# Performance work log

Measured on AMD Instinct MI355X. Metric: run time of the kernel, lower is better.

## Reference

```python
import jax, jax.numpy as jnp
import numpy as np

N, E, F_IN, H, C = 50000, 800000, 128, 64, 10

def setup_inputs() -> dict:
    key = jax.random.key(0)
    ks = jax.random.split(key, 8)
    x = jax.random.normal(ks[0], (N, F_IN), dtype=jnp.float32)
    edge_index = jax.random.randint(ks[1], (2, E), 0, N, dtype=jnp.int32)
    edge_weight = jax.random.uniform(ks[2], (E,), dtype=jnp.float32)
    W1 = jax.random.normal(ks[3], (H, F_IN), dtype=jnp.float32) * 0.05
    W2 = jax.random.normal(ks[4], (H, H), dtype=jnp.float32) * 0.05
    W3 = jax.random.normal(ks[5], (C, H), dtype=jnp.float32) * 0.05
    b1 = jnp.zeros((H,), jnp.float32)
    b2 = jnp.zeros((H,), jnp.float32)
    b3 = jnp.zeros((C,), jnp.float32)
    return {"x": x, "edge_index": edge_index, "edge_weight": edge_weight,
            "W1": W1, "b1": b1, "W2": W2, "b2": b2, "W3": W3, "b3": b3}

def reference(x, edge_index, edge_weight, W1, b1, W2, b2, W3, b3):
    n = x.shape[0]
    row, col = edge_index[0], edge_index[1]
    # GCN symmetric normalization (add_self_loops=False): deg from edge weights on col
    deg = jax.ops.segment_sum(edge_weight, col, num_segments=n)  # [N]
    dinv = jnp.where(deg > 0, jax.lax.rsqrt(deg), 0.0)
    norm = dinv[row] * edge_weight * dinv[col]  # [E]

    def gcn_layer(h, W, b):
        h = h @ W.T                               # linear transform [N, out]
        msg = h[row] * norm[:, None]              # gather + scale   [E, out]
        agg = jax.ops.segment_sum(msg, col, num_segments=n)  # scatter-add [N, out]
        return agg + b

    h = gcn_layer(x, W1, b1)
    h = gcn_layer(h, W2, b2)
    logits = gcn_layer(h, W3, b3)
    soft = jax.nn.softmax(logits, axis=1)
    return logits, soft
```

## Files before the change

kernel.cpp:

```cpp
#include <hip/hip_runtime.h>
#include <hip/hip_fp16.h>

#define N_NODES 50000
#define N_EDGES 800000
#define F_IN    128
#define H_DIM   64
#define C_DIM   10
#define CPAD    16
#define CAP     48
#define BLOCK   256
#define BIN_NODES 256
#define NBINS   196
#define QN      64
#define STRIDE  4480
#define E_BLK   2048
#define ABLOCKS ((N_EDGES + E_BLK - 1) / E_BLK)
#define GBLK    2048
#define NWAVES  (GBLK * 4)
#define POISON  ((int)0xAAAAAAAA)

__device__ __forceinline__ int unbase(int v) {
    return ((unsigned)v < 65536u) ? v : v - POISON;
}

__device__ __forceinline__ int   prow(unsigned v) { return (int)(v >> 16); }
__device__ __forceinline__ float pw(unsigned v)   {
    return __half2float(__ushort_as_half((unsigned short)(v & 0xFFFFu)));
}

__global__ __launch_bounds__(256) void k_binA(const int* __restrict__ rows,
                                              const int* __restrict__ cols,
                                              const float* __restrict__ ew,
                                              const float* __restrict__ W1,
                                              const float* __restrict__ b1,
                                              const float* __restrict__ W2,
                                              const float* __restrict__ b2,
                                              const float* __restrict__ W3,
                                              int* __restrict__ bucketCnt,
                                              unsigned* __restrict__ regionA,
                                              unsigned short* __restrict__ regionC,
                                              float* __restrict__ T2g,
                                              float* __restrict__ v1g,
                                              float* __restrict__ v2g) {
    const int tid = threadIdx.x;
    if (blockIdx.x < ABLOCKS) {
        __shared__ unsigned       sA[E_BLK];
        __shared__ unsigned short sC[E_BLK];
        __shared__ int hcnt[NBINS];
        __shared__ int lbase[NBINS];
        __shared__ int gb[NBINS];
        for (int i = tid; i < NBINS; i += BLOCK) hcnt[i] = 0;
        __syncthreads();

        const int e0 = blockIdx.x * E_BLK;
        unsigned rw[8];
        unsigned cl[8];
#pragma unroll
        for (int j = 0; j < 8; ++j) {
            int e = e0 + j * BLOCK + tid;
            if (e < N_EDGES) {
                int   c = cols[e];
                int   r = rows[e];
                float w = ew[e];
                rw[j] = ((unsigned)r << 16) | (unsigned)__half_as_ushort(__float2half(w));
                int lr = atomicAdd(&hcnt[c >> 8], 1);
                cl[j] = (unsigned)c | ((unsigned)lr << 16);
            } else {
                cl[j] = 0xFFFFFFFFu;
            }
        }
        __syncthreads();

        if (tid < 64) {
            int run = 0;
            for (int base = 0; base < NBINS; base += 64) {
                int i = base + tid;
                int v = (i < NBINS) ? hcnt[i] : 0;
                int s = v;
#pragma unroll
                for (int off = 1; off < 64; off <<= 1) {
                    int t = __shfl_up(s, off);
                    if (tid >= off) s += t;
                }
                if (i < NBINS) lbase[i] = run + s - v;
                run += __shfl(s, 63);
            }
        }
        __syncthreads();

#pragma unroll
        for (int j = 0; j < 8; ++j) {
            if (cl[j] != 0xFFFFFFFFu) {
                int c  = (int)(cl[j] & 0xFFFFu);
                int lr = (int)(cl[j] >> 16);
                int pos = lbase[c >> 8] + lr;
                sA[pos] = rw[j];
                sC[pos] = (unsigned short)c;
            }
        }
        if (tid < NBINS && hcnt[tid] > 0)
            gb[tid] = unbase(atomicAdd(&bucketCnt[tid], hcnt[tid]));
        __syncthreads();

        const int total = lbase[NBINS - 1] + hcnt[NBINS - 1];
        for (int i = tid; i < total; i += BLOCK) {
            int c = sC[i];
            int b = c >> 8;
            int gpos = gb[b] + (i - lbase[b]);
            if (gpos < STRIDE) {
                size_t p = (size_t)b * STRIDE + gpos;
                regionA[p] = sA[i];
                regionC[p] = (unsigned short)c;
            }
        }
        return;
    }

    __shared__ float u[C_DIM * H_DIM];
    for (int idx = tid; idx < C_DIM * H_DIM; idx += BLOCK) {
        int c = idx >> 6, j = idx & 63;
        float a = 0.f;
#pragma unroll
        for (int k = 0; k < H_DIM; ++k) a += W3[c * H_DIM + k] * W2[k * H_DIM + j];
        u[idx] = a;
    }
    __syncthreads();
    for (int idx = tid; idx < C_DIM * F_IN; idx += BLOCK) {
        int c = idx >> 7, f = idx & 127;
        float a = 0.f;
#pragma unroll
        for (int k = 0; k < H_DIM; ++k) a += u[c * H_DIM + k] * W1[k * F_IN + f];
        T2g[idx] = a;
    }
    if (tid < C_DIM) {
        float a = 0.f, b = 0.f;
#pragma unroll
        for (int k = 0; k < H_DIM; ++k) {
            a += u[tid * H_DIM + k] * b1[k];
            b += W3[tid * H_DIM + k] * b2[k];
        }
        v1g[tid] = a;
        v2g[tid] = b;
    }
}

__global__ __launch_bounds__(256) void k_binB(const int* __restrict__ bucketCnt,
                                              const unsigned* __restrict__ regionA,
                                              const unsigned short* __restrict__ regionC,
                                              const float* __restrict__ x,
                                              const float* __restrict__ T2g,
                                              float2* __restrict__ meta,
                                              unsigned* __restrict__ edata,
                                              __half* __restrict__ bufA) {
    __shared__ unsigned sdata[QN * CAP];
    __shared__ int   lcnt[QN];
    __shared__ float wsum[QN];
    __shared__ float dinvs[QN];
    __shared__ float ts[16 * 132];
    __shared__ float xs[16][132];
    const int tid = threadIdx.x;
    const int b   = blockIdx.x >> 2;
    const int q   = blockIdx.x & 3;
    const int n0  = b * BIN_NODES + q * QN;
    if (n0 >= N_NODES) return;
    if (tid < QN) { lcnt[tid] = 0; wsum[tid] = 0.f; }
    for (int i = tid; i < 16 * F_IN; i += BLOCK) {
        int c = i >> 7;
        ts[c * 132 + (i & 127)] = (c < C_DIM) ? T2g[i] : 0.f;
    }
    __syncthreads();

    int tot = unbase(bucketCnt[b]);
    if (tot > STRIDE) tot = STRIDE;
    const size_t segBase = (size_t)b * STRIDE;
    const int lo = q * QN, hi = lo + QN;
    for (int i = tid; i < tot; i += BLOCK) {
        int cl = (int)regionC[segBase + i] - b * BIN_NODES;
        unsigned e = regionA[segBase + i];
        if (cl >= lo && cl < hi) {
            int nl = cl - lo;
            int r = atomicAdd(&lcnt[nl], 1);
            if (r < CAP) sdata[nl * CAP + r] = e;
            atomicAdd(&wsum[nl], pw(e));
        }
    }
    __syncthreads();

    const int nvalid = min(N_NODES - n0, QN);
    if (tid < nvalid) {
        int c0 = min(lcnt[tid], CAP);
        int cp = (c0 + 15) & ~15;
        if (cp > CAP) cp = CAP;
        for (int r = c0; r < cp; ++r) sdata[tid * CAP + r] = 0u;
        float d = wsum[tid];
        float di = d > 0.f ? rsqrtf(d) : 0.f;
        dinvs[tid] = di;
        meta[n0 + tid] = make_float2(di, (float)cp);
    }
    __syncthreads();

    {
        int4* dst = reinterpret_cast<int4*>(edata + (size_t)n0 * CAP);
        const int4* src = reinterpret_cast<const int4*>(sdata);
        const int nvec = nvalid * (CAP / 4);
        for (int i = tid; i < nvec; i += BLOCK) dst[i] = src[i];
    }

    const int g = tid >> 4, c = tid & 15;
    for (int t = 0; t < QN / 16; ++t) {
        __syncthreads();
        const int n0t = n0 + t * 16;
        for (int i = tid; i < 16 * 32; i += BLOCK) {
            int ln = i >> 5, f4 = i & 31;
            if (n0t + ln < N_NODES) {
                float4 v = reinterpret_cast<const float4*>(x)[(n0t + ln) * 32 + f4];
                *reinterpret_cast<float4*>(&xs[ln][f4 * 4]) = v;
            }
        }
        __syncthreads();
        const int n = n0t + g;
        if (n < N_NODES) {
            const float di = dinvs[t * 16 + g];
            const float4* tsv = reinterpret_cast<const float4*>(&ts[c * 132]);
            const float4* xv  = reinterpret_cast<const float4*>(&xs[g][0]);
            float a = 0.f;
#pragma unroll 8
            for (int f4 = 0; f4 < 32; ++f4) {
                float4 xx = xv[f4], tt = tsv[f4];
                a += xx.x * tt.x + xx.y * tt.y + xx.z * tt.z + xx.w * tt.w;
            }
            float outv = (c < C_DIM) ? a * di : (c == 10 ? di : 0.f);
            bufA[n * CPAD + c] = __float2half(outv);
        }
    }
}

__global__ __launch_bounds__(256) void k_gather(const float2* __restrict__ meta,
                                                const unsigned* __restrict__ edata,
                                                const __half* __restrict__ zin,
                                                __half* __restrict__ zout) {
    const int lane = threadIdx.x & 63;
    const int sub = lane >> 3;
    const int c2  = lane & 7;
    const int w0 = (blockIdx.x * 256 + threadIdx.x) >> 6;
    for (int n = w0; n < N_NODES; n += NWAVES) {
        float2 m = meta[n];
        const float di = m.x;
        const int iters = ((int)m.y) >> 4;
        const uint2* bp = reinterpret_cast<const uint2*>(edata + n * CAP) + sub;
        float ax = 0.f, ay = 0.f;
#pragma unroll
        for (int i = 0; i < 3; ++i) {
            if (i < iters) {
                uint2 e = bp[i * 8];
                {
                    float2 z = __half22float2(
                        reinterpret_cast<const __half2*>(zin + prow(e.x) * CPAD)[c2]);
                    float w = pw(e.x);
                    ax += w * z.x; ay += w * z.y;
                }
                {
                    float2 z = __half22float2(
                        reinterpret_cast<const __half2*>(zin + prow(e.y) * CPAD)[c2]);
                    float w = pw(e.y);
                    ax += w * z.x; ay += w * z.y;
                }
            }
        }
        ax += __shfl_xor(ax, 8);  ay += __shfl_xor(ay, 8);
        ax += __shfl_xor(ax, 16); ay += __shfl_xor(ay, 16);
        ax += __shfl_xor(ax, 32); ay += __shfl_xor(ay, 32);
        if (lane < 8) {
            float s = di * di;
            reinterpret_cast<__half2*>(zout + n * CPAD)[lane] =
                __floats2half2_rn(ax * s, ay * s);
        }
    }
}

__global__ __launch_bounds__(256) void k_final(const float2* __restrict__ meta,
                                               const unsigned* __restrict__ edata,
                                               const __half* __restrict__ zin,
                                               const __half* __restrict__ s1buf,
                                               const float* __restrict__ v1,
                                               const float* __restrict__ v2,
                                               const float* __restrict__ b3,
                                               float* __restrict__ logits,
                                               float* __restrict__ soft) {
    const int lane = threadIdx.x & 63;
    const int sub = lane >> 3;
    const int c2  = lane & 7;
    const int w0 = (blockIdx.x * 256 + threadIdx.x) >> 6;
    for (int n = w0; n < N_NODES; n += NWAVES) {
        float2 m = meta[n];
        const float di = m.x;
        const int iters = ((int)m.y) >> 4;
        const uint2* bp = reinterpret_cast<const uint2*>(edata + n * CAP) + sub;
        float ax = 0.f, ay = 0.f;
#pragma unroll
        for (int i = 0; i < 3; ++i) {
            if (i < iters) {
                uint2 e = bp[i * 8];
                {
                    float2 z = __half22float2(
                        reinterpret_cast<const __half2*>(zin + prow(e.x) * CPAD)[c2]);
                    float w = pw(e.x);
                    ax += w * z.x; ay += w * z.y;
                }
                {
                    float2 z = __half22float2(
                        reinterpret_cast<const __half2*>(zin + prow(e.y) * CPAD)[c2]);
                    float w = pw(e.y);
                    ax += w * z.x; ay += w * z.y;
                }
            }
        }
        ax += __shfl_xor(ax, 8);  ay += __shfl_xor(ay, 8);
        ax += __shfl_xor(ax, 16); ay += __shfl_xor(ay, 16);
        ax += __shfl_xor(ax, 32); ay += __shfl_xor(ay, 32);

        const float r  = di > 0.f ? 1.0f / di : 0.f;
        const float a1 = __half2float(s1buf[n * CPAD + 10]) * r;
        const float a2 = __half2float(zin[n * CPAD + 10]) * r;
        float l0 = -1e30f, l1 = -1e30f;
        if (c2 < 5) {
            float2 w1 = reinterpret_cast<const float2*>(v1)[c2];
            float2 w2 = reinterpret_cast<const float2*>(v2)[c2];
            float2 bb = reinterpret_cast<const float2*>(b3)[c2];
            l0 = di * ax + a2 * w1.x + a1 * w2.x + bb.x;
            l1 = di * ay + a2 * w1.y + a1 * w2.y + bb.y;
        }
        float mx = fmaxf(l0, l1);
        mx = fmaxf(mx, __shfl_xor(mx, 1));
        mx = fmaxf(mx, __shfl_xor(mx, 2));
        mx = fmaxf(mx, __shfl_xor(mx, 4));
        float e0 = (c2 < 5) ? __expf(l0 - mx) : 0.f;
        float e1 = (c2 < 5) ? __expf(l1 - mx) : 0.f;
        float s = e0 + e1;
        s += __shfl_xor(s, 1);
        s += __shfl_xor(s, 2);
        s += __shfl_xor(s, 4);
        if (lane < 5) {
            float inv = 1.0f / s;
            reinterpret_cast<float2*>(logits + (size_t)n * C_DIM)[lane] = make_float2(l0, l1);
            reinterpret_cast<float2*>(soft   + (size_t)n * C_DIM)[lane] = make_float2(e0 * inv, e1 * inv);
        }
    }
}

extern "C" void kernel_launch(void* const* d_in, const int* in_sizes, int n_in,
                              void* d_out, int out_size, void* d_ws, size_t ws_size,
                              hipStream_t stream) {
    const float* x  = (const float*)d_in[0];
    const int*   ei = (const int*)d_in[1];
    const float* ew = (const float*)d_in[2];
    const float* W1 = (const float*)d_in[3];
    const float* b1 = (const float*)d_in[4];
    const float* W2 = (const float*)d_in[5];
    const float* b2 = (const float*)d_in[6];
    const float* W3 = (const float*)d_in[7];
    const float* b3 = (const float*)d_in[8];
    const int* rows = ei;
    const int* cols = ei + N_EDGES;

    char* ws = (char*)d_ws;
    size_t off = 0;
    auto alloc = [&](size_t bytes) { void* q = ws + off; off += (bytes + 15) & ~size_t(15); return q; };

    float2*         meta      = (float2*)         alloc((size_t)N_NODES * 8);
    __half*         bufA      = (__half*)         alloc((size_t)N_NODES * CPAD * 2);
    __half*         bufB      = (__half*)         alloc((size_t)N_NODES * CPAD * 2);
    float*          T2g       = (float*)          alloc(C_DIM * F_IN * 4);
    float*          v1        = (float*)          alloc(64);
    float*          v2        = (float*)          alloc(64);
    int*            bucketCnt = (int*)            alloc(NBINS * 4);
    unsigned*       regionA   = (unsigned*)       alloc((size_t)NBINS * STRIDE * 4);
    unsigned short* regionC   = (unsigned short*) alloc((size_t)NBINS * STRIDE * 2);
    unsigned*       edata     = (unsigned*)       alloc((size_t)N_NODES * CAP * 4);

    float* logits = (float*)d_out;
    float* soft   = logits + N_NODES * C_DIM;

    k_binA<<<ABLOCKS + 1, BLOCK, 0, stream>>>(rows, cols, ew, W1, b1, W2, b2, W3,
                                              bucketCnt, regionA, regionC, T2g, v1, v2);
    k_binB<<<NBINS * 4, BLOCK, 0, stream>>>(bucketCnt, regionA, regionC, x, T2g,
                                            meta, edata, bufA);
    k_gather<<<GBLK, BLOCK, 0, stream>>>(meta, edata, bufA, bufB);
    k_gather<<<GBLK, BLOCK, 0, stream>>>(meta, edata, bufB, bufA);
    k_final<<<GBLK, BLOCK, 0, stream>>>(meta, edata, bufA, bufB, v1, v2, b3,
                                        logits, soft);
}
```

Measured before the change: 163.0 us.

## Bin edges directly into 64-node sub-buckets to avoid redundant bucket scans

The edge binning pass now partitions edges into 782 buckets of 64 destination nodes instead of 196 buckets of 256 nodes, using a block-wide scan over the larger histogram. Each binB block then reads only its own bucket rather than scanning a 256-node bucket and discarding three quarters of the entries, which cuts the redundant regionA/regionC reads by four times. In exchange the per-block histogram, scan and global atomics in binA grow roughly fourfold, and the smaller per-bucket capacity of 1280 raises the risk of overflow on skewed degree distributions.

```diff
diff --git a/kernel.cpp b/kernel.cpp
--- a/kernel.cpp
+++ b/kernel.cpp
@@ -9,10 +9,9 @@
 #define CPAD    16
 #define CAP     48
 #define BLOCK   256
-#define BIN_NODES 256
-#define NBINS   196
 #define QN      64
-#define STRIDE  4480
+#define NSUB    ((N_NODES + QN - 1) / QN)
+#define SSTRIDE 1280
 #define E_BLK   2048
 #define ABLOCKS ((N_EDGES + E_BLK - 1) / E_BLK)
 #define GBLK    2048
@@ -46,10 +45,11 @@
     if (blockIdx.x < ABLOCKS) {
         __shared__ unsigned       sA[E_BLK];
         __shared__ unsigned short sC[E_BLK];
-        __shared__ int hcnt[NBINS];
-        __shared__ int lbase[NBINS];
-        __shared__ int gb[NBINS];
-        for (int i = tid; i < NBINS; i += BLOCK) hcnt[i] = 0;
+        __shared__ int hcnt[NSUB];
+        __shared__ int lbase[NSUB];
+        __shared__ int gb[NSUB];
+        __shared__ int wtot[4];
+        for (int i = tid; i < NSUB; i += BLOCK) hcnt[i] = 0;
         __syncthreads();
 
         const int e0 = blockIdx.x * E_BLK;
@@ -63,7 +63,7 @@
                 int   r = rows[e];
                 float w = ew[e];
                 rw[j] = ((unsigned)r << 16) | (unsigned)__half_as_ushort(__float2half(w));
-                int lr = atomicAdd(&hcnt[c >> 8], 1);
+                int lr = atomicAdd(&hcnt[c >> 6], 1);
                 cl[j] = (unsigned)c | ((unsigned)lr << 16);
             } else {
                 cl[j] = 0xFFFFFFFFu;
@@ -71,21 +71,30 @@
         }
         __syncthreads();
 
-        if (tid < 64) {
-            int run = 0;
-            for (int base = 0; base < NBINS; base += 64) {
-                int i = base + tid;
-                int v = (i < NBINS) ? hcnt[i] : 0;
-                int s = v;
-#pragma unroll
-                for (int off = 1; off < 64; off <<= 1) {
-                    int t = __shfl_up(s, off);
-                    if (tid >= off) s += t;
-                }
-                if (i < NBINS) lbase[i] = run + s - v;
-                run += __shfl(s, 63);
-            }
-        }
+        const int lane = tid & 63, wid = tid >> 6;
+        const int b4 = tid << 2;
+        int h0 = (b4 + 0 < NSUB) ? hcnt[b4 + 0] : 0;
+        int h1 = (b4 + 1 < NSUB) ? hcnt[b4 + 1] : 0;
+        int h2 = (b4 + 2 < NSUB) ? hcnt[b4 + 2] : 0;
+        int h3 = (b4 + 3 < NSUB) ? hcnt[b4 + 3] : 0;
+        int ls = h0 + h1 + h2 + h3;
+        int incl = ls;
+#pragma unroll
+        for (int off = 1; off < 64; off <<= 1) {
+            int t = __shfl_up(incl, off);
+            if (lane >= off) incl += t;
+        }
+        if (lane == 63) wtot[wid] = incl;
+        __syncthreads();
+        int woff = 0;
+#pragma unroll
+        for (int w = 0; w < 4; ++w) if (w < wid) woff += wtot[w];
+        int run = woff + incl - ls;
+        if (b4 + 0 < NSUB) { lbase[b4 + 0] = run; run += h0; }
+        if (b4 + 1 < NSUB) { lbase[b4 + 1] = run; run += h1; }
+        if (b4 + 2 < NSUB) { lbase[b4 + 2] = run; run += h2; }
+        if (b4 + 3 < NSUB) { lbase[b4 + 3] = run; run += h3; }
+        const int total = wtot[0] + wtot[1] + wtot[2] + wtot[3];
         __syncthreads();
 
 #pragma unroll
@@ -93,22 +102,21 @@
             if (cl[j] != 0xFFFFFFFFu) {
                 int c  = (int)(cl[j] & 0xFFFFu);
                 int lr = (int)(cl[j] >> 16);
-                int pos = lbase[c >> 8] + lr;
+                int pos = lbase[c >> 6] + lr;
                 sA[pos] = rw[j];
                 sC[pos] = (unsigned short)c;
             }
         }
-        if (tid < NBINS && hcnt[tid] > 0)
-            gb[tid] = unbase(atomicAdd(&bucketCnt[tid], hcnt[tid]));
-        __syncthreads();
-
-        const int total = lbase[NBINS - 1] + hcnt[NBINS - 1];
+        for (int i = tid; i < NSUB; i += BLOCK)
+            if (hcnt[i] > 0) gb[i] = unbase(atomicAdd(&bucketCnt[i], hcnt[i]));
+        __syncthreads();
+
         for (int i = tid; i < total; i += BLOCK) {
             int c = sC[i];
-            int b = c >> 8;
-            int gpos = gb[b] + (i - lbase[b]);
-            if (gpos < STRIDE) {
-                size_t p = (size_t)b * STRIDE + gpos;
+            int s = c >> 6;
+            int gpos = gb[s] + (i - lbase[s]);
+            if (gpos < SSTRIDE) {
+                size_t p = (size_t)s * SSTRIDE + gpos;
                 regionA[p] = sA[i];
                 regionC[p] = (unsigned short)c;
             }
@@ -159,9 +167,8 @@
     __shared__ float ts[16 * 132];
     __shared__ float xs[16][132];
     const int tid = threadIdx.x;
-    const int b   = blockIdx.x >> 2;
-    const int q   = blockIdx.x & 3;
-    const int n0  = b * BIN_NODES + q * QN;
+    const int s   = blockIdx.x;
+    const int n0  = s * QN;
     if (n0 >= N_NODES) return;
     if (tid < QN) { lcnt[tid] = 0; wsum[tid] = 0.f; }
     for (int i = tid; i < 16 * F_IN; i += BLOCK) {
@@ -170,19 +177,15 @@
     }
     __syncthreads();
 
-    int tot = unbase(bucketCnt[b]);
-    if (tot > STRIDE) tot = STRIDE;
-    const size_t segBase = (size_t)b * STRIDE;
-    const int lo = q * QN, hi = lo + QN;
+    int tot = unbase(bucketCnt[s]);
+    if (tot > SSTRIDE) tot = SSTRIDE;
+    const size_t segBase = (size_t)s * SSTRIDE;
     for (int i = tid; i < tot; i += BLOCK) {
-        int cl = (int)regionC[segBase + i] - b * BIN_NODES;
         unsigned e = regionA[segBase + i];
-        if (cl >= lo && cl < hi) {
-            int nl = cl - lo;
-            int r = atomicAdd(&lcnt[nl], 1);
-            if (r < CAP) sdata[nl * CAP + r] = e;
-            atomicAdd(&wsum[nl], pw(e));
-        }
+        int nl = (int)regionC[segBase + i] & (QN - 1);
+        int r = atomicAdd(&lcnt[nl], 1);
+        if (r < CAP) sdata[nl * CAP + r] = e;
+        atomicAdd(&wsum[nl], pw(e));
     }
     __syncthreads();
 
@@ -271,9 +274,9 @@
         ax += __shfl_xor(ax, 16); ay += __shfl_xor(ay, 16);
         ax += __shfl_xor(ax, 32); ay += __shfl_xor(ay, 32);
         if (lane < 8) {
-            float s = di * di;
+            float sc = di * di;
             reinterpret_cast<__half2*>(zout + n * CPAD)[lane] =
-                __floats2half2_rn(ax * s, ay * s);
+                __floats2half2_rn(ax * sc, ay * sc);
         }
     }
 }
@@ -336,12 +339,12 @@
         mx = fmaxf(mx, __shfl_xor(mx, 4));
         float e0 = (c2 < 5) ? __expf(l0 - mx) : 0.f;
         float e1 = (c2 < 5) ? __expf(l1 - mx) : 0.f;
-        float s = e0 + e1;
-        s += __shfl_xor(s, 1);
-        s += __shfl_xor(s, 2);
-        s += __shfl_xor(s, 4);
+        float ss = e0 + e1;
+        ss += __shfl_xor(ss, 1);
+        ss += __shfl_xor(ss, 2);
+        ss += __shfl_xor(ss, 4);
         if (lane < 5) {
-            float inv = 1.0f / s;
+            float inv = 1.0f / ss;
             reinterpret_cast<float2*>(logits + (size_t)n * C_DIM)[lane] = make_float2(l0, l1);
             reinterpret_cast<float2*>(soft   + (size_t)n * C_DIM)[lane] = make_float2(e0 * inv, e1 * inv);
         }
@@ -373,9 +376,9 @@
     float*          T2g       = (float*)          alloc(C_DIM * F_IN * 4);
     float*          v1        = (float*)          alloc(64);
     float*          v2        = (float*)          alloc(64);
-    int*            bucketCnt = (int*)            alloc(NBINS * 4);
-    unsigned*       regionA   = (unsigned*)       alloc((size_t)NBINS * STRIDE * 4);
-    unsigned short* regionC   = (unsigned short*) alloc((size_t)NBINS * STRIDE * 2);
+    int*            bucketCnt = (int*)            alloc(NSUB * 4);
+    unsigned*       regionA   = (unsigned*)       alloc((size_t)NSUB * SSTRIDE * 4);
+    unsigned short* regionC   = (unsigned short*) alloc((size_t)NSUB * SSTRIDE * 2);
     unsigned*       edata     = (unsigned*)       alloc((size_t)N_NODES * CAP * 4);
 
     float* logits = (float*)d_out;
@@ -383,8 +386,8 @@
 
     k_binA<<<ABLOCKS + 1, BLOCK, 0, stream>>>(rows, cols, ew, W1, b1, W2, b2, W3,
                                               bucketCnt, regionA, regionC, T2g, v1, v2);
-    k_binB<<<NBINS * 4, BLOCK, 0, stream>>>(bucketCnt, regionA, regionC, x, T2g,
-                                            meta, edata, bufA);
+    k_binB<<<NSUB, BLOCK, 0, stream>>>(bucketCnt, regionA, regionC, x, T2g,
+                                       meta, edata, bufA);
     k_gather<<<GBLK, BLOCK, 0, stream>>>(meta, edata, bufA, bufB);
     k_gather<<<GBLK, BLOCK, 0, stream>>>(meta, edata, bufB, bufA);
     k_final<<<GBLK, BLOCK, 0, stream>>>(meta, edata, bufA, bufB, v1, v2, b3,
```

Result: no change. 163.7 us (median of 2 runs) (+0.4%).
